# Performance work log

Measured on AMD Instinct MI355X. Metric: run time of the kernel, lower is better.

Reference implementation:

```python
import jax, jax.numpy as jnp
import numpy as np

B, S, D = 2, 2048, 768
H = 12
HD = D // H  # 64
SCALE = HD ** -0.5


def setup_inputs() -> dict:
    key = jax.random.key(0)
    k1, k2, k3, k4, k5 = jax.random.split(key, 5)
    x = jax.random.normal(k1, (B, S, D), dtype=jnp.float32)
    w_qkv = jax.random.normal(k2, (D, 3 * D), dtype=jnp.float32) * (D ** -0.5)
    b_qkv = jax.random.normal(k3, (3 * D,), dtype=jnp.float32) * 0.02
    w_proj = jax.random.normal(k4, (D, D), dtype=jnp.float32) * (D ** -0.5)
    b_proj = jax.random.normal(k5, (D,), dtype=jnp.float32) * 0.02
    return {"x": x, "w_qkv": w_qkv, "b_qkv": b_qkv, "w_proj": w_proj, "b_proj": b_proj}


def reference(x, w_qkv, b_qkv, w_proj, b_proj):
    b, s, d = x.shape
    # QKV projection: (B,S,3D) -> (3,B,H,S,HD)
    qkv = x @ w_qkv + b_qkv
    qkv = qkv.reshape(b, s, 3, H, HD).transpose(2, 0, 3, 1, 4)
    q, k, v = qkv[0], qkv[1], qkv[2]
    q = q * SCALE
    # full NxN attention scores, as in the original module
    attn = jnp.einsum("bhqd,bhkd->bhqk", q, k)
    attn = jax.nn.softmax(attn, axis=-1)
    out = jnp.einsum("bhqk,bhkd->bhqd", attn, v)  # (B,H,S,HD)
    out = out.transpose(0, 2, 1, 3).reshape(b, s, d)
    return out @ w_proj + b_proj
```

## Files before the change

### kernel.cpp

```cpp
#include <hip/hip_runtime.h>
#include <hip/hip_bf16.h>

#define B_ 2
#define S_ 2048
#define D_ 768
#define H_ 12
#define HD_ 64
#define EXP2C_ 0.1803368801111244f

typedef __attribute__((ext_vector_type(8))) short bf16x8;
typedef __attribute__((ext_vector_type(8))) unsigned short u16x8;
typedef __attribute__((ext_vector_type(4))) float f32x4;
typedef __attribute__((ext_vector_type(4))) unsigned int u32x4;

static __device__ __forceinline__ unsigned short f2bf(float x) {
    union { float f; unsigned u; } v; v.f = x;
    unsigned r = (v.u + 0x7FFFu + ((v.u >> 16) & 1u)) >> 16;
    return (unsigned short)r;
}
static __device__ __forceinline__ float bf2f(unsigned short h) {
    union { unsigned u; float f; } v; v.u = ((unsigned)h) << 16;
    return v.f;
}
static __device__ __forceinline__ float fexp2(float x) {
#if __has_builtin(__builtin_amdgcn_exp2f)
    return __builtin_amdgcn_exp2f(x);
#else
    float r; asm("v_exp_f32 %0, %1" : "=v"(r) : "v"(x)); return r;
#endif
}

static __device__ __forceinline__ unsigned pk_bf16(float a, float b) {
    __hip_bfloat162 pk = __float22bfloat162_rn(make_float2(a, b));
    union { __hip_bfloat162 h; unsigned u; } v; v.h = pk;
    return v.u;
}

static __device__ __forceinline__ f32x4 mfma32(bf16x8 a, bf16x8 b, f32x4 c) {
    return __builtin_amdgcn_mfma_f32_16x16x32_bf16(a, b, c, 0, 0, 0);
}

typedef __attribute__((address_space(3))) unsigned int lds_u32;
typedef __attribute__((address_space(1))) const unsigned int glb_u32;
static __device__ __forceinline__ void glds16(const unsigned short* g, unsigned short* l) {
    __builtin_amdgcn_global_load_lds((glb_u32*)g, (lds_u32*)l, 16, 0, 0);
}

#define PREP_CONV_ 1536
#define PREP_TQKV_ 1728
#define PREP_TPRJ_ 576
__global__ __launch_bounds__(256) void prep_kernel(
    const float* __restrict__ x,      unsigned short* __restrict__ x16,
    const float* __restrict__ w_qkv,  unsigned short* __restrict__ wqkvT,
    const float* __restrict__ w_proj, unsigned short* __restrict__ wprojT)
{
    __shared__ float tile[32][33];
    const int bid = blockIdx.x, t = threadIdx.x;
    if (bid < PREP_CONV_) {
        const int i = (bid * 256 + t) * 8;
        float4 a0 = *(const float4*)(x + i);
        float4 a1 = *(const float4*)(x + i + 4);
        u16x8 s;
        s[0] = f2bf(a0.x); s[1] = f2bf(a0.y); s[2] = f2bf(a0.z); s[3] = f2bf(a0.w);
        s[4] = f2bf(a1.x); s[5] = f2bf(a1.y); s[6] = f2bf(a1.z); s[7] = f2bf(a1.w);
        *(u16x8*)(x16 + i) = s;
        return;
    }
    const float* w; unsigned short* wT; int N, bb;
    if (bid < PREP_CONV_ + PREP_TQKV_) { w = w_qkv; wT = wqkvT; N = 3 * D_; bb = bid - PREP_CONV_; }
    else                               { w = w_proj; wT = wprojT; N = D_;   bb = bid - PREP_CONV_ - PREP_TQKV_; }
    const int K = D_;
    const int nt = N / 32;
    const int n0 = (bb % nt) * 32, k0 = (bb / nt) * 32;
    const int tx = t & 31, ty = t >> 5;
#pragma unroll
    for (int i = 0; i < 4; i++)
        tile[ty + i * 8][tx] = w[(size_t)(k0 + ty + i * 8) * N + n0 + tx];
    __syncthreads();
#pragma unroll
    for (int i = 0; i < 4; i++)
        wT[(size_t)(n0 + ty + i * 8) * K + k0 + tx] = f2bf(tile[tx][ty + i * 8]);
}

template <int BM, int BN, bool OUT_F32, bool VSPLIT>
__global__ __launch_bounds__(256) void gemm_bt_kernel(
    const unsigned short* __restrict__ A,
    const unsigned short* __restrict__ Bt,
    const float* __restrict__ bias,
    void* __restrict__ Cp,
    unsigned short* __restrict__ vt,
    int M, int N, int K)
{
    constexpr int BK = 64;
    __shared__ __align__(16) unsigned short As[BM][BK];
    __shared__ __align__(16) unsigned short Bs[BN][BK];
    constexpr int MI = BM / 32, NJ = BN / 32;
    constexpr int ACH = BM * BK / 8;
    constexpr int BCH = BN * BK / 8;

    const int t = threadIdx.x;
    const int w = t >> 6, lane = t & 63, quad = lane >> 4, l16 = lane & 15;
    const int n0 = blockIdx.x * BN, m0 = blockIdx.y * BM;
    const int mw = (w & 1) * (BM / 2), nw = (w >> 1) * (BN / 2);

    const f32x4 z = {0.f, 0.f, 0.f, 0.f};
    f32x4 acc[MI][NJ];
#pragma unroll
    for (int i = 0; i < MI; i++)
#pragma unroll
        for (int j = 0; j < NJ; j++) acc[i][j] = z;

    for (int kk = 0; kk < K; kk += BK) {
#pragma unroll
        for (int it = 0; it < ACH / 256; it++) {
            const int c = t + it * 256;
            const int row = c >> 3, gs = (c & 7) ^ (row & 7);
            glds16(A + (size_t)(m0 + row) * K + kk + gs * 8, &As[0][0] + c * 8);
        }
#pragma unroll
        for (int it = 0; it < BCH / 256; it++) {
            const int c = t + it * 256;
            const int row = c >> 3, gs = (c & 7) ^ (row & 7);
            glds16(Bt + (size_t)(n0 + row) * K + kk + gs * 8, &Bs[0][0] + c * 8);
        }
        __syncthreads();

#pragma unroll
        for (int k2 = 0; k2 < 2; k2++) {
            bf16x8 a[MI], b[NJ];
#pragma unroll
            for (int i = 0; i < MI; i++) {
                const int row = mw + i * 16 + l16;
                const int p = (quad + k2 * 4) ^ (row & 7);
                a[i] = *(const bf16x8*)(&As[row][p * 8]);
            }
#pragma unroll
            for (int j = 0; j < NJ; j++) {
                const int row = nw + j * 16 + l16;
                const int p = (quad + k2 * 4) ^ (row & 7);
                b[j] = *(const bf16x8*)(&Bs[row][p * 8]);
            }
#pragma unroll
            for (int i = 0; i < MI; i++)
#pragma unroll
                for (int j = 0; j < NJ; j++)
                    acc[i][j] = mfma32(a[i], b[j], acc[i][j]);
        }
        __syncthreads();
    }

    if (VSPLIT && n0 >= 2 * D_) {
#pragma unroll
        for (int j = 0; j < NJ; j++) {
            const int gcol = n0 + nw + j * 16 + l16;
            const int col = gcol - 2 * D_;
            const int hh = col >> 6, hd = col & 63;
            const float bv = bias[gcol];
#pragma unroll
            for (int i = 0; i < MI; i++) {
                const int row = m0 + mw + i * 16 + quad * 4;
                const int bb = row >> 11, ss = row & 2047;
                unsigned long long pkv = 0;
#pragma unroll
                for (int r = 0; r < 4; r++)
                    pkv |= (unsigned long long)f2bf(acc[i][j][r] + bv) << (16 * r);
                *(unsigned long long*)(vt +
                    ((size_t)(bb * H_ + hh) * HD_ + hd) * S_ + ss) = pkv;
            }
        }
        return;
    }

#pragma unroll
    for (int j = 0; j < NJ; j++) {
        const int col = n0 + nw + j * 16 + l16;
        const float bv = bias[col];
#pragma unroll
        for (int i = 0; i < MI; i++) {
#pragma unroll
            for (int r = 0; r < 4; r++) {
                const int row = m0 + mw + i * 16 + quad * 4 + r;
                const float v = acc[i][j][r] + bv;
                if (OUT_F32) ((float*)Cp)[(size_t)row * N + col] = v;
                else         ((unsigned short*)Cp)[(size_t)row * N + col] = f2bf(v);
            }
        }
    }
}

__global__ __launch_bounds__(256) void attn_kernel(
    const unsigned short* __restrict__ qkv,
    const unsigned short* __restrict__ vt,
    unsigned short* __restrict__ o)
{
    __shared__ __align__(16) unsigned short Ks[3][64][64];
    __shared__ __align__(16) unsigned short Vs[3][64][64];

    const int t = threadIdx.x;
    const int w = t >> 6, lane = t & 63, quad = lane >> 4, l16 = lane & 15;
    const int h8 = l16 & 7;
    const int id = blockIdx.x;
    const int xcd = id & 7, ix = id >> 3;
    const int bh = xcd * 3 + (ix >> 5);
    const int qt = ix & 31;
    const int b = bh / H_, h = bh % H_;
    const int ld = 3 * D_;

    const unsigned short* qbase =
        qkv + (size_t)(b * S_ + qt * 64 + 16 * w + l16) * ld + h * HD_;
    u16x8 qr0 = *(const u16x8*)(qbase + quad * 8);
    u16x8 qr1 = *(const u16x8*)(qbase + 32 + quad * 8);
    bf16x8 qf0, qf1;
#pragma unroll
    for (int j = 0; j < 8; j++) {
        qf0[j] = (short)f2bf(bf2f(qr0[j]) * EXP2C_);
        qf1[j] = (short)f2bf(bf2f(qr1[j]) * EXP2C_);
    }

    bf16x8 ones;
#pragma unroll
    for (int j = 0; j < 8; j++) ones[j] = (short)0x3F80;

    const unsigned short* kbase = qkv + (size_t)(b * S_) * ld + D_ + h * HD_;
    const unsigned short* vbase = vt + (size_t)bh * HD_ * S_;

    const int c0 = t, c1 = t + 256;
    const int row0 = c0 >> 3, row1 = c1 >> 3;
    const int kg0 = (c0 & 7) ^ ((row0 & 3) | (((row0 >> 3) & 1) << 2));
    const int kg1 = (c1 & 7) ^ ((row1 & 3) | (((row1 >> 3) & 1) << 2));
    const int vg0 = (c0 & 7) ^ (row0 & 7);
    const int vg1 = (c1 & 7) ^ (row1 & 7);
    const unsigned short* kp0 = kbase + (size_t)row0 * ld + kg0 * 8;
    const unsigned short* kp1 = kbase + (size_t)row1 * ld + kg1 * 8;
    const unsigned short* vp0 = vbase + (size_t)row0 * S_ + vg0 * 8;
    const unsigned short* vp1 = vbase + (size_t)row1 * S_ + vg1 * 8;
    const size_t KSTEP = (size_t)64 * ld;

    const f32x4 z = {0.f, 0.f, 0.f, 0.f};
    f32x4 o_acc[4] = {z, z, z, z};
    f32x4 l_acc = z;

#pragma unroll
    for (int pt = 0; pt < 2; pt++) {
        glds16(kp0, &Ks[pt][0][0] + c0 * 8);
        glds16(kp1, &Ks[pt][0][0] + c1 * 8);
        glds16(vp0, &Vs[pt][0][0] + c0 * 8);
        glds16(vp1, &Vs[pt][0][0] + c1 * 8);
        kp0 += KSTEP; kp1 += KSTEP; vp0 += 64; vp1 += 64;
    }
    asm volatile("s_waitcnt vmcnt(4)" ::: "memory");
    __builtin_amdgcn_s_barrier();

    const int NT = S_ / 64;
    int bc = 0;
    for (int kt = 0; kt < NT; kt++) {
        const bool pre = (kt + 2 < NT);

        if (pre) {
            const int bp = (bc + 2 >= 3) ? bc - 1 : bc + 2;
            unsigned short* kd = &Ks[bp][0][0];
            unsigned short* vd = &Vs[bp][0][0];
            glds16(kp0, kd + c0 * 8);
            glds16(kp1, kd + c1 * 8);
            glds16(vp0, vd + c0 * 8);
            glds16(vp1, vd + c1 * 8);
            kp0 += KSTEP; kp1 += KSTEP; vp0 += 64; vp1 += 64;
        }

        f32x4 s_acc[4] = {z, z, z, z};
#pragma unroll
        for (int nt = 0; nt < 4; nt++) {
            const int rowp = ((nt >> 1) << 5) + ((l16 >> 2) << 3) + ((nt & 1) << 2) + (l16 & 3);
            const int skr = (rowp & 3) | (((rowp >> 3) & 1) << 2);
            const unsigned short* kr = &Ks[bc][rowp][0];
            bf16x8 k0 = *(const bf16x8*)(kr + (quad ^ skr) * 8);
            bf16x8 k1 = *(const bf16x8*)(kr + ((quad ^ skr) ^ 4) * 8);
            s_acc[nt] = mfma32(k0, qf0, s_acc[nt]);
            s_acc[nt] = mfma32(k1, qf1, s_acc[nt]);
        }

        bf16x8 vr0[4], vr1[4];
#pragma unroll
        for (int nt = 0; nt < 4; nt++) {
            const int row = nt * 16 + l16;
            vr0[nt] = *(const bf16x8*)(&Vs[bc][row][(quad ^ h8) * 8]);
            vr1[nt] = *(const bf16x8*)(&Vs[bc][row][((quad ^ h8) ^ 4) * 8]);
        }

        f32x4 pr[4];
#pragma unroll
        for (int nt = 0; nt < 4; nt++) {
#pragma unroll
            for (int r = 0; r < 4; r++) pr[nt][r] = fexp2(s_acc[nt][r]);
        }
        union { u32x4 u; bf16x8 h; } ca, cb;
        ca.u[0] = pk_bf16(pr[0][0], pr[0][1]);
        ca.u[1] = pk_bf16(pr[0][2], pr[0][3]);
        ca.u[2] = pk_bf16(pr[1][0], pr[1][1]);
        ca.u[3] = pk_bf16(pr[1][2], pr[1][3]);
        cb.u[0] = pk_bf16(pr[2][0], pr[2][1]);
        cb.u[1] = pk_bf16(pr[2][2], pr[2][3]);
        cb.u[2] = pk_bf16(pr[3][0], pr[3][1]);
        cb.u[3] = pk_bf16(pr[3][2], pr[3][3]);
        const bf16x8 pa0 = ca.h, pa1 = cb.h;

        l_acc = mfma32(pa0, ones, l_acc);
        l_acc = mfma32(pa1, ones, l_acc);

#pragma unroll
        for (int nt = 0; nt < 4; nt++) {
            o_acc[nt] = mfma32(pa0, vr0[nt], o_acc[nt]);
            o_acc[nt] = mfma32(pa1, vr1[nt], o_acc[nt]);
        }

        if (pre) asm volatile("s_waitcnt vmcnt(4)" ::: "memory");
        else     asm volatile("s_waitcnt vmcnt(0)" ::: "memory");
        __builtin_amdgcn_s_barrier();
        bc = (bc + 1 == 3) ? 0 : bc + 1;
    }

#pragma unroll
    for (int r = 0; r < 4; r++) {
        const float inv = 1.f / l_acc[r];
        const int row = b * S_ + qt * 64 + 16 * w + quad * 4 + r;
        unsigned short* ob = o + (size_t)row * D_ + h * HD_;
#pragma unroll
        for (int nt = 0; nt < 4; nt++)
            ob[nt * 16 + l16] = f2bf(o_acc[nt][r] * inv);
    }
}

extern "C" void kernel_launch(void* const* d_in, const int* in_sizes, int n_in,
                              void* d_out, int out_size, void* d_ws, size_t ws_size,
                              hipStream_t stream) {
    const float* x      = (const float*)d_in[0];
    const float* w_qkv  = (const float*)d_in[1];
    const float* b_qkv  = (const float*)d_in[2];
    const float* w_proj = (const float*)d_in[3];
    const float* b_proj = (const float*)d_in[4];
    float* out = (float*)d_out;

    unsigned short* qkv    = (unsigned short*)d_ws;
    unsigned short* vtb    = qkv    + (size_t)(B_ * S_) * (3 * D_);
    unsigned short* o_x16  = vtb    + (size_t)(B_ * H_) * HD_ * S_;
    unsigned short* wqkvT  = o_x16  + (size_t)(B_ * S_) * D_;
    unsigned short* wprojT = wqkvT  + (size_t)D_ * (3 * D_);

    dim3 blk(256);
    prep_kernel<<<dim3(PREP_CONV_ + PREP_TQKV_ + PREP_TPRJ_), blk, 0, stream>>>(
        x, o_x16, w_qkv, wqkvT, w_proj, wprojT);
    gemm_bt_kernel<128, 96, false, true><<<dim3((3 * D_) / 96, (B_ * S_) / 128), blk, 0, stream>>>(
        o_x16, wqkvT, b_qkv, qkv, vtb, B_ * S_, 3 * D_, D_);
    attn_kernel<<<dim3((S_ / 64) * (B_ * H_)), blk, 0, stream>>>(qkv, vtb, o_x16);
    gemm_bt_kernel<64, 64, true, false><<<dim3(D_ / 64, (B_ * S_) / 64), blk, 0, stream>>>(
        o_x16, wprojT, b_proj, out, nullptr, B_ * S_, D_, D_);
}
```

Before: 149.9 us.

## Remap GEMM blocks per XCD and add triple-buffered output projection GEMM

```diff
diff --git a/kernel.cpp b/kernel.cpp
--- a/kernel.cpp
+++ b/kernel.cpp
@@ -82,7 +82,7 @@
         wT[(size_t)(n0 + ty + i * 8) * K + k0 + tx] = f2bf(tile[tx][ty + i * 8]);
 }
 
-template <int BM, int BN, bool OUT_F32, bool VSPLIT>
+template <int BM, int BN, int NBX, int MPX, bool OUT_F32, bool VSPLIT>
 __global__ __launch_bounds__(256) void gemm_bt_kernel(
     const unsigned short* __restrict__ A,
     const unsigned short* __restrict__ Bt,
@@ -100,7 +100,10 @@
 
     const int t = threadIdx.x;
     const int w = t >> 6, lane = t & 63, quad = lane >> 4, l16 = lane & 15;
-    const int n0 = blockIdx.x * BN, m0 = blockIdx.y * BM;
+    const int id = blockIdx.x;
+    const int xcd = id & 7, ix = id >> 3;
+    const int m0 = (xcd * MPX + ix / NBX) * BM;
+    const int n0 = (ix % NBX) * BN;
     const int mw = (w & 1) * (BM / 2), nw = (w >> 1) * (BN / 2);
 
     const f32x4 z = {0.f, 0.f, 0.f, 0.f};
@@ -183,6 +186,97 @@
                 const float v = acc[i][j][r] + bv;
                 if (OUT_F32) ((float*)Cp)[(size_t)row * N + col] = v;
                 else         ((unsigned short*)Cp)[(size_t)row * N + col] = f2bf(v);
+            }
+        }
+    }
+}
+
+__global__ __launch_bounds__(256) void gemm2_kernel(
+    const unsigned short* __restrict__ A,
+    const unsigned short* __restrict__ Bt,
+    const float* __restrict__ bias,
+    float* __restrict__ out)
+{
+    __shared__ __align__(16) unsigned short As[3][64][64];
+    __shared__ __align__(16) unsigned short Bs[3][64][64];
+
+    const int t = threadIdx.x;
+    const int w = t >> 6, lane = t & 63, quad = lane >> 4, l16 = lane & 15;
+    const int id = blockIdx.x;
+    const int xcd = id & 7, ix = id >> 3;
+    const int m0 = (xcd * 8 + ix / 12) * 64;
+    const int n0 = (ix % 12) * 64;
+    const int mw = (w & 1) * 32, nw = (w >> 1) * 32;
+
+    const int r0 = t >> 3, g0 = (t & 7) ^ (r0 & 7);
+    const int c1 = t + 256, r1 = c1 >> 3, g1 = (c1 & 7) ^ (r1 & 7);
+    const unsigned short* a0p = A + (size_t)(m0 + r0) * D_ + g0 * 8;
+    const unsigned short* a1p = A + (size_t)(m0 + r1) * D_ + g1 * 8;
+    const unsigned short* b0p = Bt + (size_t)(n0 + r0) * D_ + g0 * 8;
+    const unsigned short* b1p = Bt + (size_t)(n0 + r1) * D_ + g1 * 8;
+
+    auto stage = [&](int bi, int kk) {
+        glds16(a0p + kk, &As[bi][0][0] + t * 8);
+        glds16(a1p + kk, &As[bi][0][0] + (t + 256) * 8);
+        glds16(b0p + kk, &Bs[bi][0][0] + t * 8);
+        glds16(b1p + kk, &Bs[bi][0][0] + (t + 256) * 8);
+    };
+
+    const f32x4 z = {0.f, 0.f, 0.f, 0.f};
+    f32x4 acc[2][2] = {{z, z}, {z, z}};
+
+    stage(0, 0);
+    stage(1, 64);
+    asm volatile("s_waitcnt vmcnt(4)" ::: "memory");
+    __builtin_amdgcn_s_barrier();
+
+    const int NK = D_ / 64;
+    int bc = 0;
+    for (int kk = 0; kk < NK; kk++) {
+        const bool pre = (kk + 2 < NK);
+        if (pre) {
+            const int bp = (bc + 2 >= 3) ? bc - 1 : bc + 2;
+            stage(bp, (kk + 2) * 64);
+        }
+
+#pragma unroll
+        for (int k2 = 0; k2 < 2; k2++) {
+            bf16x8 a[2], b[2];
+#pragma unroll
+            for (int i = 0; i < 2; i++) {
+                const int row = mw + i * 16 + l16;
+                const int p = (quad + k2 * 4) ^ (row & 7);
+                a[i] = *(const bf16x8*)(&As[bc][row][p * 8]);
+            }
+#pragma unroll
+            for (int j = 0; j < 2; j++) {
+                const int row = nw + j * 16 + l16;
+                const int p = (quad + k2 * 4) ^ (row & 7);
+                b[j] = *(const bf16x8*)(&Bs[bc][row][p * 8]);
+            }
+#pragma unroll
+            for (int i = 0; i < 2; i++)
+#pragma unroll
+                for (int j = 0; j < 2; j++)
+                    acc[i][j] = mfma32(a[i], b[j], acc[i][j]);
+        }
+
+        if (pre) asm volatile("s_waitcnt vmcnt(4)" ::: "memory");
+        else     asm volatile("s_waitcnt vmcnt(0)" ::: "memory");
+        __builtin_amdgcn_s_barrier();
+        bc = (bc + 1 == 3) ? 0 : bc + 1;
+    }
+
+#pragma unroll
+    for (int j = 0; j < 2; j++) {
+        const int col = n0 + nw + j * 16 + l16;
+        const float bv = bias[col];
+#pragma unroll
+        for (int i = 0; i < 2; i++) {
+#pragma unroll
+            for (int r = 0; r < 4; r++) {
+                const int row = m0 + mw + i * 16 + quad * 4 + r;
+                out[(size_t)row * D_ + col] = acc[i][j][r] + bv;
             }
         }
     }
@@ -349,9 +443,8 @@
     dim3 blk(256);
     prep_kernel<<<dim3(PREP_CONV_ + PREP_TQKV_ + PREP_TPRJ_), blk, 0, stream>>>(
         x, o_x16, w_qkv, wqkvT, w_proj, wprojT);
-    gemm_bt_kernel<128, 96, false, true><<<dim3((3 * D_) / 96, (B_ * S_) / 128), blk, 0, stream>>>(
+    gemm_bt_kernel<128, 96, 24, 4, false, true><<<dim3(768), blk, 0, stream>>>(
         o_x16, wqkvT, b_qkv, qkv, vtb, B_ * S_, 3 * D_, D_);
     attn_kernel<<<dim3((S_ / 64) * (B_ * H_)), blk, 0, stream>>>(qkv, vtb, o_x16);
-    gemm_bt_kernel<64, 64, true, false><<<dim3(D_ / 64, (B_ * S_) / 64), blk, 0, stream>>>(
-        o_x16, wprojT, b_proj, out, nullptr, B_ * S_, D_, D_);
-}
+    gemm2_kernel<<<dim3(768), blk, 0, stream>>>(o_x16, wprojT, b_proj, out);
+}
```

Measured after the change: 152.0 us. About the same (+1.4%).

## Split attention KV tile across wave pairs and reduce partial outputs through LDS

Applied to the files above, without the earlier changes.

```diff
diff --git a/kernel.cpp b/kernel.cpp
--- a/kernel.cpp
+++ b/kernel.cpp
@@ -198,7 +198,7 @@
 
     const int t = threadIdx.x;
     const int w = t >> 6, lane = t & 63, quad = lane >> 4, l16 = lane & 15;
-    const int h8 = l16 & 7;
+    const int wq = w & 1, wk = w >> 1;
     const int id = blockIdx.x;
     const int xcd = id & 7, ix = id >> 3;
     const int bh = xcd * 3 + (ix >> 5);
@@ -206,15 +206,18 @@
     const int b = bh / H_, h = bh % H_;
     const int ld = 3 * D_;
 
-    const unsigned short* qbase =
-        qkv + (size_t)(b * S_ + qt * 64 + 16 * w + l16) * ld + h * HD_;
-    u16x8 qr0 = *(const u16x8*)(qbase + quad * 8);
-    u16x8 qr1 = *(const u16x8*)(qbase + 32 + quad * 8);
-    bf16x8 qf0, qf1;
-#pragma unroll
-    for (int j = 0; j < 8; j++) {
-        qf0[j] = (short)f2bf(bf2f(qr0[j]) * EXP2C_);
-        qf1[j] = (short)f2bf(bf2f(qr1[j]) * EXP2C_);
+    bf16x8 qf[2][2];
+#pragma unroll
+    for (int qs = 0; qs < 2; qs++) {
+        const unsigned short* qb =
+            qkv + (size_t)(b * S_ + qt * 64 + wq * 32 + qs * 16 + l16) * ld + h * HD_;
+#pragma unroll
+        for (int kh = 0; kh < 2; kh++) {
+            u16x8 qr = *(const u16x8*)(qb + kh * 32 + quad * 8);
+#pragma unroll
+            for (int j = 0; j < 8; j++)
+                qf[qs][kh][j] = (short)f2bf(bf2f(qr[j]) * EXP2C_);
+        }
     }
 
     bf16x8 ones;
@@ -237,8 +240,12 @@
     const size_t KSTEP = (size_t)64 * ld;
 
     const f32x4 z = {0.f, 0.f, 0.f, 0.f};
-    f32x4 o_acc[4] = {z, z, z, z};
-    f32x4 l_acc = z;
+    f32x4 o_acc[2][4];
+#pragma unroll
+    for (int qs = 0; qs < 2; qs++)
+#pragma unroll
+        for (int dg = 0; dg < 4; dg++) o_acc[qs][dg] = z;
+    f32x4 l_acc[2] = {z, z};
 
 #pragma unroll
     for (int pt = 0; pt < 2; pt++) {
@@ -267,50 +274,54 @@
             kp0 += KSTEP; kp1 += KSTEP; vp0 += 64; vp1 += 64;
         }
 
-        f32x4 s_acc[4] = {z, z, z, z};
-#pragma unroll
-        for (int nt = 0; nt < 4; nt++) {
-            const int rowp = ((nt >> 1) << 5) + ((l16 >> 2) << 3) + ((nt & 1) << 2) + (l16 & 3);
-            const int skr = (rowp & 3) | (((rowp >> 3) & 1) << 2);
-            const unsigned short* kr = &Ks[bc][rowp][0];
-            bf16x8 k0 = *(const bf16x8*)(kr + (quad ^ skr) * 8);
-            bf16x8 k1 = *(const bf16x8*)(kr + ((quad ^ skr) ^ 4) * 8);
-            s_acc[nt] = mfma32(k0, qf0, s_acc[nt]);
-            s_acc[nt] = mfma32(k1, qf1, s_acc[nt]);
-        }
-
-        bf16x8 vr0[4], vr1[4];
-#pragma unroll
-        for (int nt = 0; nt < 4; nt++) {
-            const int row = nt * 16 + l16;
-            vr0[nt] = *(const bf16x8*)(&Vs[bc][row][(quad ^ h8) * 8]);
-            vr1[nt] = *(const bf16x8*)(&Vs[bc][row][((quad ^ h8) ^ 4) * 8]);
-        }
-
-        f32x4 pr[4];
-#pragma unroll
-        for (int nt = 0; nt < 4; nt++) {
-#pragma unroll
-            for (int r = 0; r < 4; r++) pr[nt][r] = fexp2(s_acc[nt][r]);
-        }
-        union { u32x4 u; bf16x8 h; } ca, cb;
-        ca.u[0] = pk_bf16(pr[0][0], pr[0][1]);
-        ca.u[1] = pk_bf16(pr[0][2], pr[0][3]);
-        ca.u[2] = pk_bf16(pr[1][0], pr[1][1]);
-        ca.u[3] = pk_bf16(pr[1][2], pr[1][3]);
-        cb.u[0] = pk_bf16(pr[2][0], pr[2][1]);
-        cb.u[1] = pk_bf16(pr[2][2], pr[2][3]);
-        cb.u[2] = pk_bf16(pr[3][0], pr[3][1]);
-        cb.u[3] = pk_bf16(pr[3][2], pr[3][3]);
-        const bf16x8 pa0 = ca.h, pa1 = cb.h;
-
-        l_acc = mfma32(pa0, ones, l_acc);
-        l_acc = mfma32(pa1, ones, l_acc);
-
-#pragma unroll
-        for (int nt = 0; nt < 4; nt++) {
-            o_acc[nt] = mfma32(pa0, vr0[nt], o_acc[nt]);
-            o_acc[nt] = mfma32(pa1, vr1[nt], o_acc[nt]);
+        f32x4 s_acc[2][2];
+        bf16x8 kf[2][2];
+#pragma unroll
+        for (int nt = 0; nt < 2; nt++) {
+            const int rowL = ((l16 >> 2) << 3) + (nt << 2) + (l16 & 3);
+            const int row = wk * 32 + rowL;
+            const int skr = (row & 3) | (((row >> 3) & 1) << 2);
+            const unsigned short* kr = &Ks[bc][row][0];
+            kf[nt][0] = *(const bf16x8*)(kr + (quad ^ skr) * 8);
+            kf[nt][1] = *(const bf16x8*)(kr + ((quad | 4) ^ skr) * 8);
+        }
+#pragma unroll
+        for (int nt = 0; nt < 2; nt++)
+#pragma unroll
+            for (int qs = 0; qs < 2; qs++) {
+                s_acc[nt][qs] = mfma32(kf[nt][0], qf[qs][0], z);
+                s_acc[nt][qs] = mfma32(kf[nt][1], qf[qs][1], s_acc[nt][qs]);
+            }
+
+        bf16x8 vr[4];
+#pragma unroll
+        for (int dg = 0; dg < 4; dg++) {
+            const int row = dg * 16 + l16;
+            vr[dg] = *(const bf16x8*)(&Vs[bc][row][(((wk << 2) | quad) ^ (row & 7)) * 8]);
+        }
+
+        f32x4 pr[2][2];
+#pragma unroll
+        for (int nt = 0; nt < 2; nt++)
+#pragma unroll
+            for (int qs = 0; qs < 2; qs++)
+#pragma unroll
+                for (int r = 0; r < 4; r++) pr[nt][qs][r] = fexp2(s_acc[nt][qs][r]);
+        union { u32x4 u; bf16x8 h; } pku[2];
+#pragma unroll
+        for (int qs = 0; qs < 2; qs++) {
+            pku[qs].u[0] = pk_bf16(pr[0][qs][0], pr[0][qs][1]);
+            pku[qs].u[1] = pk_bf16(pr[0][qs][2], pr[0][qs][3]);
+            pku[qs].u[2] = pk_bf16(pr[1][qs][0], pr[1][qs][1]);
+            pku[qs].u[3] = pk_bf16(pr[1][qs][2], pr[1][qs][3]);
+        }
+
+#pragma unroll
+        for (int qs = 0; qs < 2; qs++) {
+            l_acc[qs] = mfma32(pku[qs].h, ones, l_acc[qs]);
+#pragma unroll
+            for (int dg = 0; dg < 4; dg++)
+                o_acc[qs][dg] = mfma32(pku[qs].h, vr[dg], o_acc[qs][dg]);
         }
 
         if (pre) asm volatile("s_waitcnt vmcnt(4)" ::: "memory");
@@ -319,14 +330,37 @@
         bc = (bc + 1 == 3) ? 0 : bc + 1;
     }
 
-#pragma unroll
-    for (int r = 0; r < 4; r++) {
-        const float inv = 1.f / l_acc[r];
-        const int row = b * S_ + qt * 64 + 16 * w + quad * 4 + r;
-        unsigned short* ob = o + (size_t)row * D_ + h * HD_;
-#pragma unroll
-        for (int nt = 0; nt < 4; nt++)
-            ob[nt * 16 + l16] = f2bf(o_acc[nt][r] * inv);
+    float* oS = (float*)&Ks[0][0][0];
+    float* lS = (float*)&Vs[0][0][0];
+    if (wk == 1) {
+#pragma unroll
+        for (int qs = 0; qs < 2; qs++) {
+#pragma unroll
+            for (int r = 0; r < 4; r++) {
+                const int qloc = wq * 32 + qs * 16 + quad * 4 + r;
+#pragma unroll
+                for (int dg = 0; dg < 4; dg++)
+                    oS[qloc * 64 + dg * 16 + l16] = o_acc[qs][dg][r];
+                if (l16 == 0) lS[qloc] = l_acc[qs][r];
+            }
+        }
+    }
+    __syncthreads();
+    if (wk == 0) {
+#pragma unroll
+        for (int qs = 0; qs < 2; qs++) {
+#pragma unroll
+            for (int r = 0; r < 4; r++) {
+                const int qloc = wq * 32 + qs * 16 + quad * 4 + r;
+                const float inv = 1.f / (l_acc[qs][r] + lS[qloc]);
+                const int row = b * S_ + qt * 64 + qloc;
+                unsigned short* ob = o + (size_t)row * D_ + h * HD_;
+#pragma unroll
+                for (int dg = 0; dg < 4; dg++)
+                    ob[dg * 16 + l16] =
+                        f2bf((o_acc[qs][dg][r] + oS[qloc * 64 + dg * 16 + l16]) * inv);
+            }
+        }
     }
 }
 
```

After: 149.3 us. Within noise of the previous version (-0.4%).
